# Kernel tuning notes

Measured on AMD Instinct MI355X. Metric: run time of the kernel, lower is better.

Reference implementation:

```python
import jax, jax.numpy as jnp
import numpy as np
import math


def setup_inputs() -> dict:
    key = jax.random.key(0)
    B, L, S, H, E = 16, 1024, 1024, 8, 64
    d = H * E  # d_model = 512
    ks = jax.random.split(key, 4)
    q = jax.random.normal(ks[0], (B, L, H, E), jnp.float32)
    k = jax.random.normal(ks[1], (B, S, H, E), jnp.float32)
    v = jax.random.normal(ks[2], (B, S, H, E), jnp.float32)
    # Conv1d(d_model, 2*d_model, kernel_size=3) weights [out, in, kw]
    W = jax.random.normal(ks[3], (2 * d, d, 3), jnp.float32) * (1.0 / math.sqrt(3 * d))
    b = jnp.zeros((2 * d,), jnp.float32)
    mask = jnp.zeros((B, L, S), jnp.bool_)  # unused by the module
    return {"q": q, "k": k, "v": v, "W": W, "b": b, "mask": mask}


def _fourier_attention(q, k, v, W, b):
    B, L, H, E = q.shape
    d = H * E
    # freq_enhance: Conv1d(d, 2d, k=3, pad=1) + GLU over channel dim
    x = q.reshape(B, L, d).transpose(0, 2, 1)  # [B, d, L]
    y = jax.lax.conv_general_dilated(
        x, W, window_strides=(1,), padding=[(1, 1)],
        dimension_numbers=("NCH", "OIH", "NCH"),
    ) + b[None, :, None]  # [B, 2d, L]
    a, g = jnp.split(y, 2, axis=1)
    q2 = (a * jax.nn.sigmoid(g)).transpose(0, 2, 1).reshape(B, L, H, E)

    xq = q2.transpose(0, 2, 3, 1)  # [B,H,E,L]
    xk = k.transpose(0, 2, 3, 1)   # [B,H,E,S]
    xv = v.transpose(0, 2, 3, 1)   # [B,H,E,S]

    qf = jnp.fft.rfft(xq, axis=-1, norm="ortho")  # [B,H,E,Lf]
    kf = jnp.fft.rfft(xk, axis=-1, norm="ortho")  # [B,H,E,Sf]
    vf = jnp.fft.rfft(xv, axis=-1, norm="ortho")  # [B,H,E,Sf]

    # complex cross-frequency scores [B,H,Lf,Sf]
    s = jnp.einsum("bhex,bhey->bhxy", qf, jnp.conj(kf)) / math.sqrt(E)

    # 'softmax' branch: magnitude gating + L1 normalization, keep phase
    mag = jnp.abs(s)
    phase = jnp.angle(s)
    mag = mag * (1.0 + jax.nn.sigmoid(mag))
    attn = mag / jnp.maximum(jnp.sum(mag, axis=-1, keepdims=True), 1e-12)  # F.normalize p=1
    sc = attn * jnp.exp(1j * phase)

    of = jnp.einsum("bhxy,bhey->bhex", sc, vf)  # [B,H,E,Lf]
    out = jnp.fft.irfft(of, n=L, axis=-1, norm="ortho").transpose(0, 3, 1, 2)  # [B,L,H,E]
    return out


def reference(q, k, v, W, b, mask):
    out = _fourier_attention(q, k, v, W, b)
    return out
```

## Files before the change

kernel.cpp:

```cpp
#include <hip/hip_runtime.h>
#include <math.h>


typedef __attribute__((ext_vector_type(8))) short bf16x8;
typedef __attribute__((ext_vector_type(4))) float f32x4;

union U8 { bf16x8 v; unsigned u[4]; };

__device__ __forceinline__ unsigned short f2b(float x) {
  unsigned u = __float_as_uint(x);
  return (unsigned short)((u + 0x7FFFu + ((u >> 16) & 1u)) >> 16);
}
__device__ __forceinline__ float b2f(unsigned short h) {
  return __uint_as_float(((unsigned)h) << 16);
}

__device__ __forceinline__ void fft1024(float2* b0, float2* b1,
                                        const float2* twd, int tid) {
  float2* src = b0;
  float2* dst = b1;
#pragma unroll
  for (int st = 0; st < 10; ++st) {
    __syncthreads();
#pragma unroll
    for (int qq = 0; qq < 2; ++qq) {
      int bi = tid + qq * 256;
      int m = 1 << st;
      int j = bi >> st;
      int jm = j << st;
      float2 c0 = src[bi];
      float2 c1 = src[bi + 512];
      float2 w = twd[jm];
      float2 sum, dif, tw;
      sum.x = c0.x + c1.x; sum.y = c0.y + c1.y;
      dif.x = c0.x - c1.x; dif.y = c0.y - c1.y;
      tw.x = dif.x * w.x - dif.y * w.y;
      tw.y = dif.x * w.y + dif.y * w.x;
      dst[bi + jm] = sum;
      dst[bi + jm + m] = tw;
    }
    float2* tmp = src; src = dst; dst = tmp;
  }
  __syncthreads();
}

__global__ __launch_bounds__(256) void transpose_kernel(
    const float* __restrict__ in, float* __restrict__ out) {
  __shared__ float tile[32][33];
  int b = blockIdx.z;
  int s0 = blockIdx.x * 32;
  int c0 = blockIdx.y * 32;
  int tx = threadIdx.x & 31;
  int ty = threadIdx.x >> 5;
  const float* ip = in + (size_t)b * (1024 * 512);
  float* op = out + (size_t)b * (1024 * 512);
#pragma unroll
  for (int i = 0; i < 32; i += 8)
    tile[ty + i][tx] = ip[(size_t)(s0 + ty + i) * 512 + c0 + tx];
  __syncthreads();
#pragma unroll
  for (int i = 0; i < 32; i += 8)
    op[(size_t)(c0 + ty + i) * 1024 + s0 + tx] = tile[tx][ty + i];
}

__global__ __launch_bounds__(256) void transpose_q_split(
    const float* __restrict__ in, unsigned* __restrict__ XPhi,
    unsigned* __restrict__ XPlo) {
  __shared__ float tile[32][33];
  int b = blockIdx.z;
  int l0 = blockIdx.x * 32;
  int c0 = blockIdx.y * 32;
  int tx = threadIdx.x & 31;
  int ty = threadIdx.x >> 5;
  const float* ip = in + (size_t)b * (1024 * 512);
#pragma unroll
  for (int i = 0; i < 32; i += 8)
    tile[ty + i][tx] = ip[(size_t)(l0 + ty + i) * 512 + c0 + tx];
  __syncthreads();
  int p = threadIdx.x & 15;
  int lb = threadIdx.x >> 4;
#pragma unroll
  for (int i = 0; i < 2; ++i) {
    int ll = lb + i * 16;
    float v0 = tile[ll][2 * p];
    float v1 = tile[ll][2 * p + 1];
    unsigned short h0 = f2b(v0), h1 = f2b(v1);
    unsigned short q0 = f2b(v0 - b2f(h0)), q1 = f2b(v1 - b2f(h1));
    size_t o = ((size_t)b * 1024 + l0 + ll) * 256 + (c0 >> 1) + p;
    XPhi[o] = (unsigned)h0 | ((unsigned)h1 << 16);
    XPlo[o] = (unsigned)q0 | ((unsigned)q1 << 16);
  }
}

__global__ __launch_bounds__(256) void transpose_w_split(
    const float* __restrict__ Win, uint2* __restrict__ Wsp) {
  __shared__ float tile[32][49];
  int og0 = blockIdx.x * 32;
  int ct0 = blockIdx.y * 48;
  int tid = threadIdx.x;
#pragma unroll
  for (int i = 0; i < 6; ++i) {
    int flat = tid + i * 256;
    int og = flat / 48, ct = flat % 48;
    tile[og][ct] = Win[(size_t)(og0 + og) * 1536 + ct0 + ct];
  }
  __syncthreads();
  int ogl = tid & 31;
  int s = tid >> 5;
#pragma unroll
  for (int i = 0; i < 3; ++i) {
    int pt = s + i * 8;
    int pl = pt / 3, t = pt % 3;
    float v0 = tile[ogl][pl * 6 + t];
    float v1 = tile[ogl][pl * 6 + 3 + t];
    unsigned short h0 = f2b(v0), h1 = f2b(v1);
    unsigned short q0 = f2b(v0 - b2f(h0)), q1 = f2b(v1 - b2f(h1));
    Wsp[((size_t)(ct0 / 6 + pl) * 3 + t) * 1024 + og0 + ogl] =
        make_uint2((unsigned)h0 | ((unsigned)h1 << 16),
                   (unsigned)q0 | ((unsigned)q1 << 16));
  }
}

__global__ __launch_bounds__(256, 2) void conv_glu_mfma(
    const unsigned* __restrict__ XPhi, const unsigned* __restrict__ XPlo,
    const uint2* __restrict__ Wsp, const float* __restrict__ bias,
    float* __restrict__ q2t) {
  __shared__ unsigned Whi[3 * 64 * 18];
  __shared__ unsigned Wlo[3 * 64 * 18];

  int tid = threadIdx.x;
  int w = tid >> 6;
  int lane = tid & 63;
  int grp = lane >> 4;
  int lid = lane & 15;

  unsigned v0 = blockIdx.x;
  int xcd = (int)(v0 & 7u);
  int j = (int)(v0 >> 3);
  int b = xcd * 2 + (j >> 6);
  int rem = j & 63;
  int ca = (rem >> 2) * 32;
  int l0 = (rem & 3) * 256;

  const unsigned* xh = XPhi + (size_t)b * 1024 * 256;
  const unsigned* xl = XPlo + (size_t)b * 1024 * 256;

  f32x4 acc[4][4];
#pragma unroll
  for (int mi = 0; mi < 4; ++mi)
#pragma unroll
    for (int ni = 0; ni < 4; ++ni) acc[mi][ni] = {0.f, 0.f, 0.f, 0.f};

  for (int c0 = 0; c0 < 512; c0 += 32) {
    __syncthreads();
#pragma unroll
    for (int i = 0; i < 12; ++i) {
      int flat = tid + i * 256;
      int ogi = flat & 63;
      int r = flat >> 6;
      int t = r % 3, p = r / 3;
      int og = (ogi < 32) ? (ca + ogi) : (480 + ca + ogi);
      uint2 g = Wsp[((size_t)((c0 >> 1) + p) * 3 + t) * 1024 + og];
      Whi[(t * 64 + ogi) * 18 + p] = g.x;
      Wlo[(t * 64 + ogi) * 18 + p] = g.y;
    }
    __syncthreads();

#pragma unroll
    for (int t = 0; t < 3; ++t) {
      U8 Ah[4], Al[4];
#pragma unroll
      for (int mi = 0; mi < 4; ++mi) {
        int base = (t * 64 + mi * 16 + lid) * 18 + 4 * grp;
        uint2 h0 = *(const uint2*)&Whi[base];
        uint2 h1 = *(const uint2*)&Whi[base + 2];
        uint2 g0 = *(const uint2*)&Wlo[base];
        uint2 g1 = *(const uint2*)&Wlo[base + 2];
        Ah[mi].u[0] = h0.x; Ah[mi].u[1] = h0.y;
        Ah[mi].u[2] = h1.x; Ah[mi].u[3] = h1.y;
        Al[mi].u[0] = g0.x; Al[mi].u[1] = g0.y;
        Al[mi].u[2] = g1.x; Al[mi].u[3] = g1.y;
      }
      U8 Bh[4], Bl[4];
#pragma unroll
      for (int ni = 0; ni < 4; ++ni) {
        unsigned gl = (unsigned)(l0 + w * 64 + ni * 16 + lid + t - 1);
        uint4 dh = make_uint4(0, 0, 0, 0), dl = make_uint4(0, 0, 0, 0);
        if (gl < 1024u) {
          size_t off = (size_t)gl * 256 + (c0 >> 1) + 4 * grp;
          dh = *(const uint4*)(xh + off);
          dl = *(const uint4*)(xl + off);
        }
        Bh[ni].u[0] = dh.x; Bh[ni].u[1] = dh.y;
        Bh[ni].u[2] = dh.z; Bh[ni].u[3] = dh.w;
        Bl[ni].u[0] = dl.x; Bl[ni].u[1] = dl.y;
        Bl[ni].u[2] = dl.z; Bl[ni].u[3] = dl.w;
      }
#pragma unroll
      for (int mi = 0; mi < 4; ++mi)
#pragma unroll
        for (int ni = 0; ni < 4; ++ni) {
          acc[mi][ni] = __builtin_amdgcn_mfma_f32_16x16x32_bf16(
              Ah[mi].v, Bl[ni].v, acc[mi][ni], 0, 0, 0);
          acc[mi][ni] = __builtin_amdgcn_mfma_f32_16x16x32_bf16(
              Al[mi].v, Bh[ni].v, acc[mi][ni], 0, 0, 0);
          acc[mi][ni] = __builtin_amdgcn_mfma_f32_16x16x32_bf16(
              Ah[mi].v, Bh[ni].v, acc[mi][ni], 0, 0, 0);
        }
    }
  }

#pragma unroll
  for (int mi = 0; mi < 2; ++mi)
#pragma unroll
    for (int rr = 0; rr < 4; ++rr) {
      int row = mi * 16 + grp * 4 + rr;
      float ba = bias[ca + row];
      float bg = bias[512 + ca + row];
      float* orow =
          q2t + ((size_t)b * 512 + ca + row) * 1024 + l0 + w * 64 + lid;
#pragma unroll
      for (int ni = 0; ni < 4; ++ni) {
        float a = acc[mi][ni][rr] + ba;
        float g = acc[mi + 2][ni][rr] + bg;
        orow[ni * 16] = a / (1.f + __expf(-g));
      }
    }
}

__global__ __launch_bounds__(256) void fft_fwd_kernel(
    const float* __restrict__ in, ushort4* __restrict__ out, float scale) {
  __shared__ float2 sb0[1024];
  __shared__ float2 sb1[1024];
  __shared__ float2 twd[512];
  int tid = threadIdx.x;
  size_t r = blockIdx.x;
  const float* ip = in + r * 1024;
#pragma unroll
  for (int i = 0; i < 4; ++i) {
    int idx = tid + i * 256;
    sb0[idx] = make_float2(ip[idx], 0.f);
  }
  for (int kk = tid; kk < 512; kk += 256) {
    float ang = -6.283185307179586f * (float)kk * (1.0f / 1024.0f);
    float sn, cs;
    __sincosf(ang, &sn, &cs);
    twd[kk] = make_float2(cs, sn);
  }
  fft1024(sb0, sb1, twd, tid);
  ushort4* op = out + r * 514;
  for (int x = tid; x < 513; x += 256) {
    float2 v = sb0[x];
    float re = v.x * scale, im = v.y * scale;
    unsigned short rh = f2b(re), ih = f2b(im);
    unsigned short rl = f2b(re - b2f(rh)), il = f2b(im - b2f(ih));
    op[x] = make_ushort4(rh, ih, rl, il);
  }
  if (tid == 0) op[513] = make_ushort4(0, 0, 0, 0);
}

__global__ __launch_bounds__(256) void attn_kernel(
    const ushort4* __restrict__ qf, const ushort4* __restrict__ kf,
    const ushort4* __restrict__ vf, float2* __restrict__ of) {
  __shared__ __align__(16) unsigned char smem[49664];
  ushort4* kv = (ushort4*)smem;
  ushort4* qs = (ushort4*)(smem + 32768);
  unsigned char* Shi = smem + 32768;
  unsigned char* Slo = smem + 40960;
  float* zred = (float*)(smem + 49152);

  int tid = threadIdx.x;
  int w = tid >> 6;
  int lane = tid & 63;
  int grp = lane >> 4;
  int lid = lane & 15;

  unsigned v0 = blockIdx.x;
  unsigned cc = v0 & 7u;
  unsigned jj = v0 >> 3;
  int bh = (int)(cc + 8u * (jj / 17u));
  int x0 = (int)(jj % 17u) * 32;

  const ushort4* qb = qf + (size_t)bh * (64 * 514);
  const ushort4* kb = kf + (size_t)bh * (64 * 514);
  const ushort4* vb = vf + (size_t)bh * (64 * 514);

  {
    int x = tid & 31, e0 = tid >> 5;
    int gx = x0 + x;
#pragma unroll
    for (int i = 0; i < 8; ++i) {
      int e = e0 + i * 8;
      ushort4 qv = make_ushort4(0, 0, 0, 0);
      if (gx < 514) qv = qb[(size_t)e * 514 + gx];
      qs[e * 32 + x] = qv;
    }
  }
  __syncthreads();

  U8 Ah[2][4], Al[2][4];
#pragma unroll
  for (int mt = 0; mt < 2; ++mt)
#pragma unroll
    for (int ks = 0; ks < 4; ++ks)
#pragma unroll
      for (int jp = 0; jp < 4; ++jp) {
        ushort4 qv = qs[(ks * 16 + grp * 4 + jp) * 32 + mt * 16 + lid];
        Ah[mt][ks].u[jp] = (unsigned)qv.x | ((unsigned)qv.y << 16);
        Al[mt][ks].u[jp] = (unsigned)qv.z | ((unsigned)qv.w << 16);
      }

  float zacc[2][4] = {{0.f, 0.f, 0.f, 0.f}, {0.f, 0.f, 0.f, 0.f}};
  f32x4 ore[2] = {{0.f, 0.f, 0.f, 0.f}, {0.f, 0.f, 0.f, 0.f}};
  f32x4 oim[2] = {{0.f, 0.f, 0.f, 0.f}, {0.f, 0.f, 0.f, 0.f}};

  for (int yt = 0; yt < 9; ++yt) {
    int y0 = yt * 64;
    __syncthreads();
    {
      int yy = (tid & 31) * 2, e0 = tid >> 5;
#pragma unroll
      for (int i = 0; i < 8; ++i) {
        int e = e0 + i * 8;
        uint4 d = make_uint4(0, 0, 0, 0);
        int gy = y0 + yy;
        if (gy < 513) d = *(const uint4*)(kb + (size_t)e * 514 + gy);
        int sw = e & 7;
        *(uint2*)&kv[e * 64 + (yy ^ sw)] = make_uint2(d.x, d.y);
        *(uint2*)&kv[e * 64 + ((yy + 1) ^ sw)] = make_uint2(d.z, d.w);
      }
    }
    __syncthreads();
    {
      f32x4 cre[2] = {{0.f, 0.f, 0.f, 0.f}, {0.f, 0.f, 0.f, 0.f}};
      f32x4 cim[2] = {{0.f, 0.f, 0.f, 0.f}, {0.f, 0.f, 0.f, 0.f}};
#pragma unroll
      for (int ks = 0; ks < 4; ++ks) {
        U8 brh, brl, bih, bil;
#pragma unroll
        for (int jp = 0; jp < 4; ++jp) {
          int e = ks * 16 + grp * 4 + jp;
          ushort4 kvv = kv[e * 64 + ((w * 16 + lid) ^ (e & 7))];
          unsigned uh = (unsigned)kvv.x | ((unsigned)kvv.y << 16);
          unsigned ul = (unsigned)kvv.z | ((unsigned)kvv.w << 16);
          brh.u[jp] = uh;
          brl.u[jp] = ul;
          bih.u[jp] = ((uh >> 16) ^ 0x8000u) | (uh << 16);
          bil.u[jp] = ((ul >> 16) ^ 0x8000u) | (ul << 16);
        }
#pragma unroll
        for (int mt = 0; mt < 2; ++mt) {
          cre[mt] = __builtin_amdgcn_mfma_f32_16x16x32_bf16(Ah[mt][ks].v, brh.v, cre[mt], 0, 0, 0);
          cre[mt] = __builtin_amdgcn_mfma_f32_16x16x32_bf16(Al[mt][ks].v, brh.v, cre[mt], 0, 0, 0);
          cre[mt] = __builtin_amdgcn_mfma_f32_16x16x32_bf16(Ah[mt][ks].v, brl.v, cre[mt], 0, 0, 0);
          cim[mt] = __builtin_amdgcn_mfma_f32_16x16x32_bf16(Ah[mt][ks].v, bih.v, cim[mt], 0, 0, 0);
          cim[mt] = __builtin_amdgcn_mfma_f32_16x16x32_bf16(Al[mt][ks].v, bih.v, cim[mt], 0, 0, 0);
          cim[mt] = __builtin_amdgcn_mfma_f32_16x16x32_bf16(Ah[mt][ks].v, bil.v, cim[mt], 0, 0, 0);
        }
      }
      int ybase4 = 4 * (w * 16 + lid);
#pragma unroll
      for (int mt = 0; mt < 2; ++mt)
#pragma unroll
        for (int r = 0; r < 4; ++r) {
          float sre = cre[mt][r], sim = cim[mt][r];
          float m = sqrtf(sre * sre + sim * sim);
          float f = 1.f + 1.f / (1.f + __expf(-m));
          zacc[mt][r] += m * f;
          float wre = sre * f, wim = sim * f;
          unsigned short hr = f2b(wre), hi2 = f2b(wim);
          unsigned short lr = f2b(wre - b2f(hr)), li = f2b(wim - b2f(hi2));
          int x = mt * 16 + grp * 4 + r;
          int bc = ybase4 ^ ((x & 7) << 4);
          *(unsigned*)(Shi + x * 256 + bc) = (unsigned)hr | ((unsigned)hi2 << 16);
          *(unsigned*)(Slo + x * 256 + bc) = (unsigned)lr | ((unsigned)li << 16);
        }
    }
    __syncthreads();
    {
      int yy = (tid & 31) * 2, e0 = tid >> 5;
#pragma unroll
      for (int i = 0; i < 8; ++i) {
        int e = e0 + i * 8;
        uint4 d = make_uint4(0, 0, 0, 0);
        int gy = y0 + yy;
        if (gy < 513) d = *(const uint4*)(vb + (size_t)e * 514 + gy);
        int sw = e & 7;
        *(uint2*)&kv[e * 64 + (yy ^ sw)] = make_uint2(d.x, d.y);
        *(uint2*)&kv[e * 64 + ((yy + 1) ^ sw)] = make_uint2(d.z, d.w);
      }
    }
    __syncthreads();
    {
#pragma unroll
      for (int ks = 0; ks < 4; ++ks) {
        U8 brh, brl, bih, bil;
#pragma unroll
        for (int jp = 0; jp < 4; ++jp) {
          int e = w * 16 + lid;
          int y = ks * 16 + grp * 4 + jp;
          ushort4 vv = kv[e * 64 + (y ^ (e & 7))];
          unsigned uh = (unsigned)vv.x | ((unsigned)vv.y << 16);
          unsigned ul = (unsigned)vv.z | ((unsigned)vv.w << 16);
          brh.u[jp] = uh ^ 0x80000000u;
          brl.u[jp] = ul ^ 0x80000000u;
          bih.u[jp] = (uh >> 16) | (uh << 16);
          bil.u[jp] = (ul >> 16) | (ul << 16);
        }
#pragma unroll
        for (int mt = 0; mt < 2; ++mt) {
          int x = mt * 16 + lid;
          int bc = (ks * 64 + grp * 16) ^ ((x & 7) << 4);
          U8 a2h, a2l;
          a2h.v = *(const bf16x8*)(Shi + x * 256 + bc);
          a2l.v = *(const bf16x8*)(Slo + x * 256 + bc);
          ore[mt] = __builtin_amdgcn_mfma_f32_16x16x32_bf16(a2h.v, brh.v, ore[mt], 0, 0, 0);
          ore[mt] = __builtin_amdgcn_mfma_f32_16x16x32_bf16(a2l.v, brh.v, ore[mt], 0, 0, 0);
          ore[mt] = __builtin_amdgcn_mfma_f32_16x16x32_bf16(a2h.v, brl.v, ore[mt], 0, 0, 0);
          oim[mt] = __builtin_amdgcn_mfma_f32_16x16x32_bf16(a2h.v, bih.v, oim[mt], 0, 0, 0);
          oim[mt] = __builtin_amdgcn_mfma_f32_16x16x32_bf16(a2l.v, bih.v, oim[mt], 0, 0, 0);
          oim[mt] = __builtin_amdgcn_mfma_f32_16x16x32_bf16(a2h.v, bil.v, oim[mt], 0, 0, 0);
        }
      }
    }
  }

#pragma unroll
  for (int mt = 0; mt < 2; ++mt)
#pragma unroll
    for (int r = 0; r < 4; ++r) {
      float z = zacc[mt][r];
      z += __shfl_xor(z, 1); z += __shfl_xor(z, 2);
      z += __shfl_xor(z, 4); z += __shfl_xor(z, 8);
      zacc[mt][r] = z;
    }
  __syncthreads();
  if (lid == 0) {
#pragma unroll
    for (int mt = 0; mt < 2; ++mt)
#pragma unroll
      for (int r = 0; r < 4; ++r)
        zred[w * 32 + mt * 16 + grp * 4 + r] = zacc[mt][r];
  }
  __syncthreads();
  float2* ov = (float2*)smem;
#pragma unroll
  for (int mt = 0; mt < 2; ++mt)
#pragma unroll
    for (int r = 0; r < 4; ++r) {
      int x = mt * 16 + grp * 4 + r;
      float z = zred[x] + zred[32 + x] + zred[64 + x] + zred[96 + x];
      float inv = 1.f / fmaxf(z, 1e-12f);
      int e = w * 16 + lid;
      ov[e * 32 + (x ^ ((e & 7) << 2))] =
          make_float2(ore[mt][r] * inv, oim[mt][r] * inv);
    }
  __syncthreads();
  {
    float2* ob = of + (size_t)bh * 64 * 513;
#pragma unroll
    for (int i = 0; i < 4; ++i) {
      int e = (tid >> 4) + i * 16;
      int xq = (tid & 15) * 2;
      int sw = (e & 7) << 2;
      float2 a = ov[e * 32 + (xq ^ sw)];
      float2 b2 = ov[e * 32 + ((xq + 1) ^ sw)];
      int gx = x0 + xq;
      if (gx < 513) ob[(size_t)e * 513 + gx] = a;
      if (gx + 1 < 513) ob[(size_t)e * 513 + gx + 1] = b2;
    }
  }
}

__global__ __launch_bounds__(256) void fft_inv_kernel(
    const float2* __restrict__ in, float* __restrict__ out) {
  __shared__ float2 sb0[1024];
  __shared__ float2 sb1[1024];
  __shared__ float2 twd[512];
  int tid = threadIdx.x;
  size_t r = blockIdx.x;
  const float2* ip = in + r * 513;
#pragma unroll
  for (int i = 0; i < 4; ++i) {
    int idx = tid + i * 256;
    float2 v;
    if (idx < 513) {
      v = ip[idx];
    } else {
      float2 u = ip[1024 - idx];
      v = make_float2(u.x, -u.y);
    }
    sb0[idx] = v;
  }
  for (int kk = tid; kk < 512; kk += 256) {
    float ang = 6.283185307179586f * (float)kk * (1.0f / 1024.0f);
    float sn, cs;
    __sincosf(ang, &sn, &cs);
    twd[kk] = make_float2(cs, sn);
  }
  fft1024(sb0, sb1, twd, tid);
  int e = (int)(r & 63);
  int h = (int)((r >> 6) & 7);
  size_t b = r >> 9;
  float* op = out + b * (size_t)(1024 * 512) + (size_t)h * 64 + e;
  const float sc = 0.03125f;
#pragma unroll
  for (int i = 0; i < 4; ++i) {
    int l = tid + i * 256;
    op[(size_t)l * 512] = sb0[l].x * sc;
  }
}

extern "C" void kernel_launch(void* const* d_in, const int* in_sizes, int n_in,
                              void* d_out, int out_size, void* d_ws, size_t ws_size,
                              hipStream_t stream) {
  const float* q = (const float*)d_in[0];
  const float* k = (const float*)d_in[1];
  const float* v = (const float*)d_in[2];
  const float* W = (const float*)d_in[3];
  const float* bias = (const float*)d_in[4];
  float* out = (float*)d_out;

  float* wsf = (float*)d_ws;
  float*    A    = wsf;
  unsigned* XPhi = (unsigned*)(wsf + 8421376);
  unsigned* XPlo = XPhi + (size_t)16 * 1024 * 256;
  ushort4*  qf   = (ushort4*)(wsf + 8421376);
  uint2*    Wsp  = (uint2*)(wsf + 16842752);
  ushort4*  vf   = (ushort4*)(wsf + 16842752);
  ushort4*  kf   = (ushort4*)(wsf + 25264128);
  float2*   of   = (float2*)wsf;

  transpose_q_split<<<dim3(32, 16, 16), 256, 0, stream>>>(q, XPhi, XPlo);
  transpose_w_split<<<dim3(32, 32), 256, 0, stream>>>(W, Wsp);
  conv_glu_mfma<<<dim3(1024), 256, 0, stream>>>(XPhi, XPlo, Wsp, bias, A);
  fft_fwd_kernel<<<dim3(8192), 256, 0, stream>>>(A, qf, 0.03125f * 0.125f);
  transpose_kernel<<<dim3(32, 16, 16), 256, 0, stream>>>(k, A);
  fft_fwd_kernel<<<dim3(8192), 256, 0, stream>>>(A, kf, 0.03125f);
  transpose_kernel<<<dim3(32, 16, 16), 256, 0, stream>>>(v, A);
  fft_fwd_kernel<<<dim3(8192), 256, 0, stream>>>(A, vf, 0.03125f);
  attn_kernel<<<dim3(2176), 256, 0, stream>>>(qf, kf, vf, of);
  fft_inv_kernel<<<dim3(8192), 256, 0, stream>>>(of, out);
}
```

Baseline: 834.3 us.

## Load K/V fragments directly from global and pre-transpose V for attention

```diff
diff --git a/kernel.cpp b/kernel.cpp
--- a/kernel.cpp
+++ b/kernel.cpp
@@ -13,6 +13,11 @@
 }
 __device__ __forceinline__ float b2f(unsigned short h) {
   return __uint_as_float(((unsigned)h) << 16);
+}
+__device__ __forceinline__ unsigned cvtpk_bf16(float lo, float hi) {
+  unsigned r;
+  asm("v_cvt_pk_bf16_f32 %0, %1, %2" : "=v"(r) : "v"(lo), "v"(hi));
+  return r;
 }
 
 __device__ __forceinline__ void fft1024(float2* b0, float2* b1,
@@ -259,15 +264,144 @@
   if (tid == 0) op[513] = make_ushort4(0, 0, 0, 0);
 }
 
-__global__ __launch_bounds__(256) void attn_kernel(
-    const ushort4* __restrict__ qf, const ushort4* __restrict__ kf,
-    const ushort4* __restrict__ vf, float2* __restrict__ of) {
-  __shared__ __align__(16) unsigned char smem[49664];
-  ushort4* kv = (ushort4*)smem;
-  ushort4* qs = (ushort4*)(smem + 32768);
-  unsigned char* Shi = smem + 32768;
-  unsigned char* Slo = smem + 40960;
-  float* zred = (float*)(smem + 49152);
+__global__ __launch_bounds__(256) void vft_kernel(
+    const uint2* __restrict__ vf, uint2* __restrict__ vfT) {
+  __shared__ uint2 tile[64][65];
+  int bh = blockIdx.y;
+  int y0 = blockIdx.x * 64;
+  int tid = threadIdx.x;
+  const uint2* src = vf + (size_t)bh * 64 * 514;
+  uint2* dst = vfT + (size_t)bh * 514 * 64;
+#pragma unroll
+  for (int i = 0; i < 16; ++i) {
+    int flat = tid + i * 256;
+    int e = flat >> 6, y = flat & 63;
+    int gy = y0 + y;
+    uint2 d = make_uint2(0, 0);
+    if (gy < 514) d = src[(size_t)e * 514 + gy];
+    tile[e][y] = d;
+  }
+  __syncthreads();
+#pragma unroll
+  for (int i = 0; i < 16; ++i) {
+    int flat = tid + i * 256;
+    int y = flat >> 6, e = flat & 63;
+    int gy = y0 + y;
+    if (gy < 514) dst[(size_t)gy * 64 + e] = tile[e][y];
+  }
+}
+
+template <bool TAIL>
+__device__ __forceinline__ void attn_tile(
+    int y0, const uint2* __restrict__ kb, const uint2* __restrict__ vb,
+    const U8 (&Ah)[2][4], const U8 (&Al)[2][4],
+    unsigned* Shi, unsigned* Slo, float* zacc, f32x4* ore, f32x4* oim,
+    int w, int grp, int lid) {
+  int yk = y0 + 16 * w + lid;
+  uint2 BK[4][4];
+  bool kval = !TAIL || (yk < 514);
+#pragma unroll
+  for (int ks = 0; ks < 4; ++ks)
+#pragma unroll
+    for (int jp = 0; jp < 4; ++jp) {
+      int e = ks * 16 + grp * 4 + jp;
+      if (!TAIL) {
+        BK[ks][jp] = kb[(size_t)e * 514 + yk];
+      } else {
+        uint2 d = make_uint2(0, 0);
+        if (kval) d = kb[(size_t)e * 514 + yk];
+        BK[ks][jp] = d;
+      }
+    }
+  f32x4 cre[2] = {{0.f, 0.f, 0.f, 0.f}, {0.f, 0.f, 0.f, 0.f}};
+  f32x4 cim[2] = {{0.f, 0.f, 0.f, 0.f}, {0.f, 0.f, 0.f, 0.f}};
+#pragma unroll
+  for (int ks = 0; ks < 4; ++ks) {
+    U8 bhh, bll, bih, bil;
+#pragma unroll
+    for (int jp = 0; jp < 4; ++jp) {
+      unsigned uh = BK[ks][jp].x, ul = BK[ks][jp].y;
+      bhh.u[jp] = uh;
+      bll.u[jp] = ul;
+      bih.u[jp] = ((uh >> 16) ^ 0x8000u) | (uh << 16);
+      bil.u[jp] = ((ul >> 16) ^ 0x8000u) | (ul << 16);
+    }
+#pragma unroll
+    for (int mt = 0; mt < 2; ++mt) {
+      cre[mt] = __builtin_amdgcn_mfma_f32_16x16x32_bf16(Ah[mt][ks].v, bhh.v, cre[mt], 0, 0, 0);
+      cre[mt] = __builtin_amdgcn_mfma_f32_16x16x32_bf16(Al[mt][ks].v, bhh.v, cre[mt], 0, 0, 0);
+      cre[mt] = __builtin_amdgcn_mfma_f32_16x16x32_bf16(Ah[mt][ks].v, bll.v, cre[mt], 0, 0, 0);
+      cim[mt] = __builtin_amdgcn_mfma_f32_16x16x32_bf16(Ah[mt][ks].v, bih.v, cim[mt], 0, 0, 0);
+      cim[mt] = __builtin_amdgcn_mfma_f32_16x16x32_bf16(Al[mt][ks].v, bih.v, cim[mt], 0, 0, 0);
+      cim[mt] = __builtin_amdgcn_mfma_f32_16x16x32_bf16(Ah[mt][ks].v, bil.v, cim[mt], 0, 0, 0);
+    }
+  }
+#pragma unroll
+  for (int mt = 0; mt < 2; ++mt)
+#pragma unroll
+    for (int r = 0; r < 4; ++r) {
+      float sre = cre[mt][r], sim = cim[mt][r];
+      float m = sqrtf(sre * sre + sim * sim);
+      float f = 1.f + 1.f / (1.f + __expf(-m));
+      zacc[mt * 4 + r] += m * f;
+      float wre = sre * f, wim = sim * f;
+      unsigned dh = cvtpk_bf16(wre, wim);
+      float rre = wre - __uint_as_float(dh << 16);
+      float rim = wim - __uint_as_float(dh & 0xffff0000u);
+      unsigned dl = cvtpk_bf16(rre, rim);
+      int x = mt * 16 + grp * 4 + r;
+      int idx = x * 64 + ((16 * w + lid) ^ ((x & 15) << 2));
+      Shi[idx] = dh;
+      Slo[idx] = dl;
+    }
+  __syncthreads();
+#pragma unroll
+  for (int ks = 0; ks < 4; ++ks) {
+    uint2 BV[4];
+#pragma unroll
+    for (int jp = 0; jp < 4; ++jp) {
+      int yv = y0 + ks * 16 + grp * 4 + jp;
+      if (!TAIL) {
+        BV[jp] = vb[(size_t)yv * 64 + 16 * w + lid];
+      } else {
+        uint2 d = make_uint2(0, 0);
+        if (yv < 514) d = vb[(size_t)yv * 64 + 16 * w + lid];
+        BV[jp] = d;
+      }
+    }
+    U8 bvh, bvl, bvi, bvj;
+#pragma unroll
+    for (int jp = 0; jp < 4; ++jp) {
+      unsigned uh = BV[jp].x, ul = BV[jp].y;
+      bvh.u[jp] = uh ^ 0x80000000u;
+      bvl.u[jp] = ul ^ 0x80000000u;
+      bvi.u[jp] = (uh >> 16) | (uh << 16);
+      bvj.u[jp] = (ul >> 16) | (ul << 16);
+    }
+#pragma unroll
+    for (int mt = 0; mt < 2; ++mt) {
+      int sidx = (mt * 16 + lid) * 64 + ((ks * 16 + grp * 4) ^ (lid << 2));
+      U8 a2h, a2l;
+      a2h.v = *(const bf16x8*)&Shi[sidx];
+      a2l.v = *(const bf16x8*)&Slo[sidx];
+      ore[mt] = __builtin_amdgcn_mfma_f32_16x16x32_bf16(a2h.v, bvh.v, ore[mt], 0, 0, 0);
+      ore[mt] = __builtin_amdgcn_mfma_f32_16x16x32_bf16(a2l.v, bvh.v, ore[mt], 0, 0, 0);
+      ore[mt] = __builtin_amdgcn_mfma_f32_16x16x32_bf16(a2h.v, bvl.v, ore[mt], 0, 0, 0);
+      oim[mt] = __builtin_amdgcn_mfma_f32_16x16x32_bf16(a2h.v, bvi.v, oim[mt], 0, 0, 0);
+      oim[mt] = __builtin_amdgcn_mfma_f32_16x16x32_bf16(a2l.v, bvi.v, oim[mt], 0, 0, 0);
+      oim[mt] = __builtin_amdgcn_mfma_f32_16x16x32_bf16(a2h.v, bvj.v, oim[mt], 0, 0, 0);
+    }
+  }
+  __syncthreads();
+}
+
+__global__ __launch_bounds__(256, 3) void attn_kernel(
+    const uint2* __restrict__ qf, const uint2* __restrict__ kf,
+    const uint2* __restrict__ vfT, float2* __restrict__ of) {
+  __shared__ __align__(16) unsigned char smem[16896];
+  unsigned* Shi = (unsigned*)smem;
+  unsigned* Slo = (unsigned*)(smem + 8192);
+  float* zred = (float*)(smem + 16384);
 
   int tid = threadIdx.x;
   int w = tid >> 6;
@@ -281,166 +415,53 @@
   int bh = (int)(cc + 8u * (jj / 17u));
   int x0 = (int)(jj % 17u) * 32;
 
-  const ushort4* qb = qf + (size_t)bh * (64 * 514);
-  const ushort4* kb = kf + (size_t)bh * (64 * 514);
-  const ushort4* vb = vf + (size_t)bh * (64 * 514);
-
-  {
-    int x = tid & 31, e0 = tid >> 5;
-    int gx = x0 + x;
-#pragma unroll
-    for (int i = 0; i < 8; ++i) {
-      int e = e0 + i * 8;
-      ushort4 qv = make_ushort4(0, 0, 0, 0);
-      if (gx < 514) qv = qb[(size_t)e * 514 + gx];
-      qs[e * 32 + x] = qv;
-    }
-  }
-  __syncthreads();
+  const uint2* qb = qf + (size_t)bh * (64 * 514);
+  const uint2* kb = kf + (size_t)bh * (64 * 514);
+  const uint2* vb = vfT + (size_t)bh * (514 * 64);
 
   U8 Ah[2][4], Al[2][4];
 #pragma unroll
-  for (int mt = 0; mt < 2; ++mt)
+  for (int mt = 0; mt < 2; ++mt) {
+    int gx = x0 + mt * 16 + lid;
+    bool qv = gx < 514;
 #pragma unroll
     for (int ks = 0; ks < 4; ++ks)
 #pragma unroll
       for (int jp = 0; jp < 4; ++jp) {
-        ushort4 qv = qs[(ks * 16 + grp * 4 + jp) * 32 + mt * 16 + lid];
-        Ah[mt][ks].u[jp] = (unsigned)qv.x | ((unsigned)qv.y << 16);
-        Al[mt][ks].u[jp] = (unsigned)qv.z | ((unsigned)qv.w << 16);
+        int e = ks * 16 + grp * 4 + jp;
+        uint2 d = make_uint2(0, 0);
+        if (qv) d = qb[(size_t)e * 514 + gx];
+        Ah[mt][ks].u[jp] = d.x;
+        Al[mt][ks].u[jp] = d.y;
       }
-
-  float zacc[2][4] = {{0.f, 0.f, 0.f, 0.f}, {0.f, 0.f, 0.f, 0.f}};
+  }
+
+  float zacc[8] = {0.f, 0.f, 0.f, 0.f, 0.f, 0.f, 0.f, 0.f};
   f32x4 ore[2] = {{0.f, 0.f, 0.f, 0.f}, {0.f, 0.f, 0.f, 0.f}};
   f32x4 oim[2] = {{0.f, 0.f, 0.f, 0.f}, {0.f, 0.f, 0.f, 0.f}};
 
-  for (int yt = 0; yt < 9; ++yt) {
-    int y0 = yt * 64;
-    __syncthreads();
-    {
-      int yy = (tid & 31) * 2, e0 = tid >> 5;
-#pragma unroll
-      for (int i = 0; i < 8; ++i) {
-        int e = e0 + i * 8;
-        uint4 d = make_uint4(0, 0, 0, 0);
-        int gy = y0 + yy;
-        if (gy < 513) d = *(const uint4*)(kb + (size_t)e * 514 + gy);
-        int sw = e & 7;
-        *(uint2*)&kv[e * 64 + (yy ^ sw)] = make_uint2(d.x, d.y);
-        *(uint2*)&kv[e * 64 + ((yy + 1) ^ sw)] = make_uint2(d.z, d.w);
-      }
-    }
-    __syncthreads();
-    {
-      f32x4 cre[2] = {{0.f, 0.f, 0.f, 0.f}, {0.f, 0.f, 0.f, 0.f}};
-      f32x4 cim[2] = {{0.f, 0.f, 0.f, 0.f}, {0.f, 0.f, 0.f, 0.f}};
-#pragma unroll
-      for (int ks = 0; ks < 4; ++ks) {
-        U8 brh, brl, bih, bil;
-#pragma unroll
-        for (int jp = 0; jp < 4; ++jp) {
-          int e = ks * 16 + grp * 4 + jp;
-          ushort4 kvv = kv[e * 64 + ((w * 16 + lid) ^ (e & 7))];
-          unsigned uh = (unsigned)kvv.x | ((unsigned)kvv.y << 16);
-          unsigned ul = (unsigned)kvv.z | ((unsigned)kvv.w << 16);
-          brh.u[jp] = uh;
-          brl.u[jp] = ul;
-          bih.u[jp] = ((uh >> 16) ^ 0x8000u) | (uh << 16);
-          bil.u[jp] = ((ul >> 16) ^ 0x8000u) | (ul << 16);
-        }
-#pragma unroll
-        for (int mt = 0; mt < 2; ++mt) {
-          cre[mt] = __builtin_amdgcn_mfma_f32_16x16x32_bf16(Ah[mt][ks].v, brh.v, cre[mt], 0, 0, 0);
-          cre[mt] = __builtin_amdgcn_mfma_f32_16x16x32_bf16(Al[mt][ks].v, brh.v, cre[mt], 0, 0, 0);
-          cre[mt] = __builtin_amdgcn_mfma_f32_16x16x32_bf16(Ah[mt][ks].v, brl.v, cre[mt], 0, 0, 0);
-          cim[mt] = __builtin_amdgcn_mfma_f32_16x16x32_bf16(Ah[mt][ks].v, bih.v, cim[mt], 0, 0, 0);
-          cim[mt] = __builtin_amdgcn_mfma_f32_16x16x32_bf16(Al[mt][ks].v, bih.v, cim[mt], 0, 0, 0);
-          cim[mt] = __builtin_amdgcn_mfma_f32_16x16x32_bf16(Ah[mt][ks].v, bil.v, cim[mt], 0, 0, 0);
-        }
-      }
-      int ybase4 = 4 * (w * 16 + lid);
-#pragma unroll
-      for (int mt = 0; mt < 2; ++mt)
-#pragma unroll
-        for (int r = 0; r < 4; ++r) {
-          float sre = cre[mt][r], sim = cim[mt][r];
-          float m = sqrtf(sre * sre + sim * sim);
-          float f = 1.f + 1.f / (1.f + __expf(-m));
-          zacc[mt][r] += m * f;
-          float wre = sre * f, wim = sim * f;
-          unsigned short hr = f2b(wre), hi2 = f2b(wim);
-          unsigned short lr = f2b(wre - b2f(hr)), li = f2b(wim - b2f(hi2));
-          int x = mt * 16 + grp * 4 + r;
-          int bc = ybase4 ^ ((x & 7) << 4);
-          *(unsigned*)(Shi + x * 256 + bc) = (unsigned)hr | ((unsigned)hi2 << 16);
-          *(unsigned*)(Slo + x * 256 + bc) = (unsigned)lr | ((unsigned)li << 16);
-        }
-    }
-    __syncthreads();
-    {
-      int yy = (tid & 31) * 2, e0 = tid >> 5;
-#pragma unroll
-      for (int i = 0; i < 8; ++i) {
-        int e = e0 + i * 8;
-        uint4 d = make_uint4(0, 0, 0, 0);
-        int gy = y0 + yy;
-        if (gy < 513) d = *(const uint4*)(vb + (size_t)e * 514 + gy);
-        int sw = e & 7;
-        *(uint2*)&kv[e * 64 + (yy ^ sw)] = make_uint2(d.x, d.y);
-        *(uint2*)&kv[e * 64 + ((yy + 1) ^ sw)] = make_uint2(d.z, d.w);
-      }
-    }
-    __syncthreads();
-    {
-#pragma unroll
-      for (int ks = 0; ks < 4; ++ks) {
-        U8 brh, brl, bih, bil;
-#pragma unroll
-        for (int jp = 0; jp < 4; ++jp) {
-          int e = w * 16 + lid;
-          int y = ks * 16 + grp * 4 + jp;
-          ushort4 vv = kv[e * 64 + (y ^ (e & 7))];
-          unsigned uh = (unsigned)vv.x | ((unsigned)vv.y << 16);
-          unsigned ul = (unsigned)vv.z | ((unsigned)vv.w << 16);
-          brh.u[jp] = uh ^ 0x80000000u;
-          brl.u[jp] = ul ^ 0x80000000u;
-          bih.u[jp] = (uh >> 16) | (uh << 16);
-          bil.u[jp] = (ul >> 16) | (ul << 16);
-        }
-#pragma unroll
-        for (int mt = 0; mt < 2; ++mt) {
-          int x = mt * 16 + lid;
-          int bc = (ks * 64 + grp * 16) ^ ((x & 7) << 4);
-          U8 a2h, a2l;
-          a2h.v = *(const bf16x8*)(Shi + x * 256 + bc);
-          a2l.v = *(const bf16x8*)(Slo + x * 256 + bc);
-          ore[mt] = __builtin_amdgcn_mfma_f32_16x16x32_bf16(a2h.v, brh.v, ore[mt], 0, 0, 0);
-          ore[mt] = __builtin_amdgcn_mfma_f32_16x16x32_bf16(a2l.v, brh.v, ore[mt], 0, 0, 0);
-          ore[mt] = __builtin_amdgcn_mfma_f32_16x16x32_bf16(a2h.v, brl.v, ore[mt], 0, 0, 0);
-          oim[mt] = __builtin_amdgcn_mfma_f32_16x16x32_bf16(a2h.v, bih.v, oim[mt], 0, 0, 0);
-          oim[mt] = __builtin_amdgcn_mfma_f32_16x16x32_bf16(a2l.v, bih.v, oim[mt], 0, 0, 0);
-          oim[mt] = __builtin_amdgcn_mfma_f32_16x16x32_bf16(a2h.v, bil.v, oim[mt], 0, 0, 0);
-        }
-      }
-    }
-  }
+#pragma unroll 1
+  for (int yt = 0; yt < 8; ++yt)
+    attn_tile<false>(yt * 64, kb, vb, Ah, Al, Shi, Slo, zacc, ore, oim,
+                     w, grp, lid);
+  attn_tile<true>(512, kb, vb, Ah, Al, Shi, Slo, zacc, ore, oim,
+                  w, grp, lid);
 
 #pragma unroll
   for (int mt = 0; mt < 2; ++mt)
 #pragma unroll
     for (int r = 0; r < 4; ++r) {
-      float z = zacc[mt][r];
+      float z = zacc[mt * 4 + r];
       z += __shfl_xor(z, 1); z += __shfl_xor(z, 2);
       z += __shfl_xor(z, 4); z += __shfl_xor(z, 8);
-      zacc[mt][r] = z;
-    }
-  __syncthreads();
+      zacc[mt * 4 + r] = z;
+    }
   if (lid == 0) {
 #pragma unroll
     for (int mt = 0; mt < 2; ++mt)
 #pragma unroll
       for (int r = 0; r < 4; ++r)
-        zred[w * 32 + mt * 16 + grp * 4 + r] = zacc[mt][r];
+        zred[w * 32 + mt * 16 + grp * 4 + r] = zacc[mt * 4 + r];
   }
   __syncthreads();
   float2* ov = (float2*)smem;
@@ -523,13 +544,14 @@
 
   float* wsf = (float*)d_ws;
   float*    A    = wsf;
+  uint2*    vfT  = (uint2*)wsf;
   unsigned* XPhi = (unsigned*)(wsf + 8421376);
   unsigned* XPlo = XPhi + (size_t)16 * 1024 * 256;
   ushort4*  qf   = (ushort4*)(wsf + 8421376);
   uint2*    Wsp  = (uint2*)(wsf + 16842752);
   ushort4*  vf   = (ushort4*)(wsf + 16842752);
+  float2*   of   = (float2*)(wsf + 16842752);
   ushort4*  kf   = (ushort4*)(wsf + 25264128);
-  float2*   of   = (float2*)wsf;
 
   transpose_q_split<<<dim3(32, 16, 16), 256, 0, stream>>>(q, XPhi, XPlo);
   transpose_w_split<<<dim3(32, 32), 256, 0, stream>>>(W, Wsp);
@@ -539,6 +561,8 @@
   fft_fwd_kernel<<<dim3(8192), 256, 0, stream>>>(A, kf, 0.03125f);
   transpose_kernel<<<dim3(32, 16, 16), 256, 0, stream>>>(v, A);
   fft_fwd_kernel<<<dim3(8192), 256, 0, stream>>>(A, vf, 0.03125f);
-  attn_kernel<<<dim3(2176), 256, 0, stream>>>(qf, kf, vf, of);
+  vft_kernel<<<dim3(9, 128), 256, 0, stream>>>((const uint2*)vf, vfT);
+  attn_kernel<<<dim3(2176), 256, 0, stream>>>((const uint2*)qf, (const uint2*)kf,
+                                              vfT, of);
   fft_inv_kernel<<<dim3(8192), 256, 0, stream>>>(of, out);
 }
```

Result: faster. 774.3 us (-7.2%).
